# Kernel optimization log

Hardware: AMD Instinct MI355X
Metric: run time of the kernel (lower is better)

## Reference

```python
import jax, jax.numpy as jnp
import numpy as np

V, E, H = 50000, 300, 512
L, N, K = 6, 8192, 4


def setup_inputs() -> dict:
    key = jax.random.key(0)
    ks = jax.random.split(key, 12)
    vocab_ix = jax.random.randint(ks[0], (L, N), 0, V)
    child_idx = jax.random.randint(ks[1], (L, N, K), 0, N)
    token_mask = jnp.ones((L, N), dtype=jnp.float32)
    child_mask = (jax.random.uniform(ks[2], (L, N, K)) < 0.75).astype(jnp.float32)
    s = 0.02
    embed = jax.random.normal(ks[3], (V, E), dtype=jnp.float32)
    W_iou = jax.random.normal(ks[4], (E, 3 * H), dtype=jnp.float32) * s
    U_iou = jax.random.normal(ks[5], (H, 3 * H), dtype=jnp.float32) * s
    b_iou = jnp.zeros((3 * H,), dtype=jnp.float32)
    W_f = jax.random.normal(ks[6], (E, H), dtype=jnp.float32) * s
    U_f = jax.random.normal(ks[7], (H, H), dtype=jnp.float32) * s
    b_f = jnp.zeros((H,), dtype=jnp.float32)
    return {"vocab_ix": vocab_ix, "child_idx": child_idx, "token_mask": token_mask,
            "child_mask": child_mask, "embed": embed, "W_iou": W_iou, "U_iou": U_iou,
            "b_iou": b_iou, "W_f": W_f, "U_f": U_f, "b_f": b_f}


def _tree_lstm(vocab_ix, child_idx, token_mask, child_mask,
               embed, W_iou, U_iou, b_iou, W_f, U_f, b_f):
    # bottom-up over levels; level L-1 = leaves (no children -> zero prev states)
    h = jnp.zeros((N, H), dtype=embed.dtype)
    c = jnp.zeros((N, H), dtype=embed.dtype)
    for l in reversed(range(L)):
        # word2vec: embedding lookup; zero vector for non-token nodes
        x = embed[vocab_ix[l]] * token_mask[l][:, None]            # [N, E]
        xWf = x @ W_f                                              # [N, H]
        if l == L - 1:
            h_tilde = jnp.zeros((N, H), dtype=x.dtype)
            fc = jnp.zeros((N, H), dtype=x.dtype)
        else:
            m = child_mask[l][:, :, None]                          # [N, K, 1]
            h_ch = h[child_idx[l]] * m                             # [N, K, H]
            c_ch = c[child_idx[l]] * m                             # [N, K, H]
            h_tilde = h_ch.sum(axis=1)                             # child-sum
            # per-child forget gates (padded slots: c_ch is 0 -> no contribution)
            f = jax.nn.sigmoid(xWf[:, None, :] + jnp.einsum('nkh,hj->nkj', h_ch, U_f) + b_f)
            fc = (f * c_ch).sum(axis=1)
        iou = x @ W_iou + h_tilde @ U_iou + b_iou                  # [N, 3H]
        i, o, u = jnp.split(iou, 3, axis=-1)
        c = jax.nn.sigmoid(i) * jnp.tanh(u) + fc
        h = jax.nn.sigmoid(o) * jnp.tanh(c)
    return h  # outputs[0][1]: hidden states of root level


def reference(vocab_ix, child_idx, token_mask, child_mask,
              embed, W_iou, U_iou, b_iou, W_f, U_f, b_f):
    return _tree_lstm(vocab_ix, child_idx, token_mask, child_mask,
                      embed, W_iou, U_iou, b_iou, W_f, U_f, b_f)
```

## Files before the change

kernel.cpp:

```cpp
#include <hip/hip_runtime.h>
#include <cmath>

#define VSZ  50000
#define EDIM 300
#define EPAD 320
#define HDIM 512
#define LVLS 6
#define NN   8192
#define KCH  4

#define BM 128
#define BN 128
#define BK 32

typedef __attribute__((ext_vector_type(8))) short bf16x8;
typedef __attribute__((ext_vector_type(8))) unsigned short us8;
typedef __attribute__((ext_vector_type(4))) float f32x4;

__device__ __forceinline__ float sigf(float x) { return 1.0f / (1.0f + expf(-x)); }

__device__ __forceinline__ unsigned short f2bf(float f) {
    unsigned u = __float_as_uint(f);
    u += 0x7FFF + ((u >> 16) & 1);
    return (unsigned short)(u >> 16);
}
__device__ __forceinline__ float bf2f(unsigned short h) {
    return __uint_as_float(((unsigned)h) << 16);
}

__device__ __forceinline__ unsigned cvt_pk_bf16(float lo, float hi) {
    unsigned r;
    asm("v_cvt_pk_bf16_f32 %0, %1, %2" : "=v"(r) : "v"(lo), "v"(hi));
    return r;
}

__global__ __launch_bounds__(256) void gconv_k(
    const float* __restrict__ embed, const int* __restrict__ vix,
    const float* __restrict__ tmask, unsigned short* __restrict__ out)
{
    int t  = blockIdx.x * 256 + threadIdx.x;
    int r  = t / (EPAD / 8);
    int j8 = (t - r * (EPAD / 8)) * 8;
    float m = tmask[r];
    int   v = vix[r];
    const float* src = embed + (size_t)v * EDIM + j8;
    us8 o;
    if (j8 + 8 <= EDIM) {
        float4 a = *(const float4*)(src);
        float4 b = *(const float4*)(src + 4);
        const float xs[8] = {a.x, a.y, a.z, a.w, b.x, b.y, b.z, b.w};
#pragma unroll
        for (int j = 0; j < 8; ++j) o[j] = f2bf(xs[j] * m);
    } else {
#pragma unroll
        for (int j = 0; j < 8; ++j) {
            float x = (j8 + j < EDIM) ? src[j] * m : 0.0f;
            o[j] = f2bf(x);
        }
    }
    *(us8*)(out + (size_t)r * EPAD + j8) = o;
}

__global__ __launch_bounds__(256) void wconv_k(
    const float* __restrict__ in, unsigned short* __restrict__ out,
    int Kreal, int Ksp, int Nd)
{
    int t = blockIdx.x * 256 + threadIdx.x;
    int k = t % Ksp;
    int n = t / Ksp;
    out[t] = (k < Kreal) ? f2bf(in[(size_t)k * Nd + n]) : (unsigned short)0;
}

#define GLL(src, dst)                                                        \
    __builtin_amdgcn_global_load_lds(                                        \
        (const __attribute__((address_space(1))) unsigned int*)(src), (dst), 16, 0, 0)

template <int EPI, int NCHUNK>
__global__ __launch_bounds__(256) void mgemm_k(
    const unsigned short* __restrict__ Ab,
    const unsigned short* __restrict__ Bt,
    const float* __restrict__ b_iou, const float* __restrict__ b_f,
    unsigned short* __restrict__ C, int ldc, int Ks)
{
    __shared__ __align__(16) unsigned short smem[4 * BM * BK];
    unsigned short* As0 = smem;
    unsigned short* Bs0 = smem + BM * BK;
    unsigned short* As1 = smem + 2 * BM * BK;
    unsigned short* Bs1 = smem + 3 * BM * BK;

    const int tid  = threadIdx.x;
    const int wave = tid >> 6;
    const int lane = tid & 63;
    const int quad = lane >> 4;
    const int mcol = lane & 15;
    const int wm   = (wave >> 1) * 64;
    const int wn   = (wave & 1) * 64;
    const int band = wave >> 1;

    const int GX   = gridDim.x;
    const int P    = blockIdx.x + GX * blockIdx.y;
    const int g    = P & 7;
    const int s    = P >> 3;
    const int mper = gridDim.y >> 3;
    const int sdiv = s / GX;
    const int my_mt = g * mper + sdiv;
    const int my_ng = s - sdiv * GX;
    const int tile_m = my_mt * BM;

    const int r0  = tid >> 2;
    const int kg0 = (tid & 3) ^ ((r0 >> 1) & 3);
    const int cc1 = tid + 256;
    const int r1  = cc1 >> 2;
    const int kg1 = (cc1 & 3) ^ ((r1 >> 1) & 3);

    const unsigned short* asrc0 = Ab + (size_t)(tile_m + r0) * Ks + kg0 * 8;
    const unsigned short* asrc1 = Ab + (size_t)(tile_m + r1) * Ks + kg1 * 8;

    typedef __attribute__((address_space(3))) unsigned int lds_u32;
    lds_u32* dA0_0 = (lds_u32*)(As0 + wave * 512);
    lds_u32* dA1_0 = (lds_u32*)(As0 + 2048 + wave * 512);
    lds_u32* dB0_0 = (lds_u32*)(Bs0 + wave * 512);
    lds_u32* dB1_0 = (lds_u32*)(Bs0 + 2048 + wave * 512);
    lds_u32* dA0_1 = (lds_u32*)(As1 + wave * 512);
    lds_u32* dA1_1 = (lds_u32*)(As1 + 2048 + wave * 512);
    lds_u32* dB0_1 = (lds_u32*)(Bs1 + wave * 512);
    lds_u32* dB1_1 = (lds_u32*)(Bs1 + 2048 + wave * 512);

    float* eb = reinterpret_cast<float*>(smem);
    const int erl = tid >> 3;
    const int ecg = tid & 7;

#define STAGE0(kk) { GLL(asrc0 + (kk), dA0_0); GLL(asrc1 + (kk), dA1_0);    \
                     GLL(bsrc0 + (kk), dB0_0); GLL(bsrc1 + (kk), dB1_0); }
#define STAGE1(kk) { GLL(asrc0 + (kk), dA0_1); GLL(asrc1 + (kk), dA1_1);    \
                     GLL(bsrc0 + (kk), dB0_1); GLL(bsrc1 + (kk), dB1_1); }
#define WAITV4  asm volatile("s_waitcnt vmcnt(4)" ::: "memory")
#define WAITV0  asm volatile("s_waitcnt vmcnt(0)" ::: "memory")
#define BAR     __builtin_amdgcn_s_barrier()

#define COMPUTE(AS, BS)                                                     \
    {                                                                       \
        bf16x8 afr[4], bfr[4];                                              \
        _Pragma("unroll")                                                   \
        for (int mt = 0; mt < 4; ++mt) {                                    \
            int rw = wm + mt * 16 + mcol;                                   \
            int p  = rw * 4 + (quad ^ ((rw >> 1) & 3));                     \
            afr[mt] = *(const bf16x8*)((AS) + p * 8);                       \
        }                                                                   \
        _Pragma("unroll")                                                   \
        for (int nt = 0; nt < 4; ++nt) {                                    \
            int rw = wn + nt * 16 + mcol;                                   \
            int p  = rw * 4 + (quad ^ ((rw >> 1) & 3));                     \
            bfr[nt] = *(const bf16x8*)((BS) + p * 8);                       \
        }                                                                   \
        _Pragma("unroll")                                                   \
        for (int mt = 0; mt < 4; ++mt)                                      \
            _Pragma("unroll")                                               \
            for (int nt = 0; nt < 4; ++nt)                                  \
                acc[mt][nt] = __builtin_amdgcn_mfma_f32_16x16x32_bf16(      \
                    afr[mt], bfr[nt], acc[mt][nt], 0, 0, 0);                \
    }

    for (int nc = 0; nc < NCHUNK; ++nc) {
        const int tile_n = (my_ng * NCHUNK + nc) * BN;
        const unsigned short* bsrc0 = Bt + (size_t)(tile_n + r0) * Ks + kg0 * 8;
        const unsigned short* bsrc1 = Bt + (size_t)(tile_n + r1) * Ks + kg1 * 8;

        f32x4 acc[4][4] = {};
        const int nsteps = Ks / BK;

        STAGE0(0);

        for (int st = 0; st < nsteps; st += 2) {
            if (st + 1 < nsteps) { STAGE1((st + 1) * BK); WAITV4; }
            else                 { WAITV0; }
            BAR;
            COMPUTE(As0, Bs0);
            BAR;
            if (st + 2 < nsteps) { STAGE0((st + 2) * BK); WAITV4; }
            else                 { WAITV0; }
            BAR;
            COMPUTE(As1, Bs1);
            BAR;
        }

#pragma unroll
        for (int mt = 0; mt < 4; ++mt) {
            const int rbase = band * 16 + quad * 4;
#pragma unroll
            for (int nt = 0; nt < 4; ++nt) {
                const int cb = wn + nt * 16 + mcol;
                const int gq = cb >> 2;
                const int cl = cb & 3;
#pragma unroll
                for (int rr = 0; rr < 4; ++rr) {
                    const int r = rbase + rr;
                    eb[r * 128 + ((gq ^ (r & 7)) << 2) + cl] = acc[mt][nt][rr];
                }
            }
            __syncthreads();

            const int grow = tile_m + (erl >> 4) * 64 + mt * 16 + (erl & 15);
            const int gcol = tile_n + ecg * 16;
            float v[16];
#pragma unroll
            for (int sxt = 0; sxt < 4; ++sxt) {
                const int pg = (ecg * 4 + sxt) ^ (erl & 7);
                f32x4 q = *(const f32x4*)&eb[erl * 128 + pg * 4];
                v[sxt * 4 + 0] = q[0]; v[sxt * 4 + 1] = q[1];
                v[sxt * 4 + 2] = q[2]; v[sxt * 4 + 3] = q[3];
            }
            if (EPI == 1) {
                const float* bp = (gcol < 3 * HDIM) ? (b_iou + gcol)
                                                    : (b_f + gcol - 3 * HDIM);
                float4 b0 = *(const float4*)(bp);
                float4 b1 = *(const float4*)(bp + 4);
                float4 b2 = *(const float4*)(bp + 8);
                float4 b3 = *(const float4*)(bp + 12);
                const float bb[16] = {b0.x, b0.y, b0.z, b0.w, b1.x, b1.y, b1.z, b1.w,
                                      b2.x, b2.y, b2.z, b2.w, b3.x, b3.y, b3.z, b3.w};
#pragma unroll
                for (int j = 0; j < 16; ++j) v[j] += bb[j];
            }
            unsigned pw[8];
#pragma unroll
            for (int j = 0; j < 8; ++j) pw[j] = cvt_pk_bf16(v[2 * j], v[2 * j + 1]);
            unsigned short* cp = C + (size_t)grow * ldc + gcol;
            *(uint4*)(cp)     = make_uint4(pw[0], pw[1], pw[2], pw[3]);
            *(uint4*)(cp + 8) = make_uint4(pw[4], pw[5], pw[6], pw[7]);
            __syncthreads();
        }
    }
#undef STAGE0
#undef STAGE1
#undef WAITV4
#undef WAITV0
#undef BAR
#undef COMPUTE
}

template <bool LAST>
__global__ __launch_bounds__(256) void gatefc_k(
    const unsigned short* __restrict__ iouxW, const unsigned short* __restrict__ Z,
    const int* __restrict__ cidx, const float* __restrict__ cmask,
    const float* __restrict__ c_prev,
    float* __restrict__ c_new, unsigned short* __restrict__ hb_new,
    float* __restrict__ h_out)
{
    int t  = blockIdx.x * 256 + threadIdx.x;
    int n  = t >> 6;
    int j8 = (t & 63) << 3;
    const unsigned short* xr = iouxW + (size_t)n * 4 * HDIM + j8;
    us8 xi = *(const us8*)xr;
    us8 xo = *(const us8*)(xr + HDIM);
    us8 xu = *(const us8*)(xr + 2 * HDIM);
    us8 xf = *(const us8*)(xr + 3 * HDIM);
    float ia[8], oa[8], ua[8], xw[8], fc[8];
#pragma unroll
    for (int j = 0; j < 8; ++j) {
        ia[j] = bf2f(xi[j]); oa[j] = bf2f(xo[j]);
        ua[j] = bf2f(xu[j]); xw[j] = bf2f(xf[j]);
        fc[j] = 0.0f;
    }
    int4   ci = *(const int4*)&cidx[n * KCH];
    float4 cm = *(const float4*)&cmask[n * KCH];
    const int   cia[4] = {ci.x, ci.y, ci.z, ci.w};
    const float cma[4] = {cm.x, cm.y, cm.z, cm.w};
#pragma unroll
    for (int k = 0; k < KCH; ++k) {
        const float m = cma[k];
        const unsigned short* zr = Z + (size_t)cia[k] * 4 * HDIM + j8;
        us8 zi = *(const us8*)zr;
        us8 zo = *(const us8*)(zr + HDIM);
        us8 zu = *(const us8*)(zr + 2 * HDIM);
        us8 zf = *(const us8*)(zr + 3 * HDIM);
        const float* cpr = c_prev + (size_t)cia[k] * HDIM + j8;
        float4 ca = *(const float4*)cpr;
        float4 cb = *(const float4*)(cpr + 4);
        const float cp[8] = {ca.x, ca.y, ca.z, ca.w, cb.x, cb.y, cb.z, cb.w};
#pragma unroll
        for (int j = 0; j < 8; ++j) {
            ia[j] += m * bf2f(zi[j]);
            oa[j] += m * bf2f(zo[j]);
            ua[j] += m * bf2f(zu[j]);
            fc[j] += sigf(xw[j] + m * bf2f(zf[j])) * m * cp[j];
        }
    }
    float cv[8], hv[8];
#pragma unroll
    for (int j = 0; j < 8; ++j) {
        cv[j] = sigf(ia[j]) * tanhf(ua[j]) + fc[j];
        hv[j] = sigf(oa[j]) * tanhf(cv[j]);
    }
    if (LAST) {
        float4 h0 = make_float4(hv[0], hv[1], hv[2], hv[3]);
        float4 h1 = make_float4(hv[4], hv[5], hv[6], hv[7]);
        *(float4*)(h_out + (size_t)n * HDIM + j8)     = h0;
        *(float4*)(h_out + (size_t)n * HDIM + j8 + 4) = h1;
    } else {
        float4 c0v = make_float4(cv[0], cv[1], cv[2], cv[3]);
        float4 c1v = make_float4(cv[4], cv[5], cv[6], cv[7]);
        *(float4*)(c_new + (size_t)n * HDIM + j8)     = c0v;
        *(float4*)(c_new + (size_t)n * HDIM + j8 + 4) = c1v;
        us8 hb;
#pragma unroll
        for (int j = 0; j < 8; ++j) hb[j] = f2bf(hv[j]);
        *(us8*)(hb_new + (size_t)n * HDIM + j8) = hb;
    }
}

__global__ __launch_bounds__(256) void gateleaf_k(
    const unsigned short* __restrict__ iouxW,
    float* __restrict__ c_new, unsigned short* __restrict__ hb_new)
{
    int t  = blockIdx.x * 256 + threadIdx.x;
    int n  = t >> 6;
    int j8 = (t & 63) << 3;
    const unsigned short* xr = iouxW + (size_t)n * 4 * HDIM + j8;
    us8 xi = *(const us8*)xr;
    us8 xo = *(const us8*)(xr + HDIM);
    us8 xu = *(const us8*)(xr + 2 * HDIM);
    float cv[8], hv[8];
#pragma unroll
    for (int j = 0; j < 8; ++j) {
        cv[j] = sigf(bf2f(xi[j])) * tanhf(bf2f(xu[j]));
        hv[j] = sigf(bf2f(xo[j])) * tanhf(cv[j]);
    }
    float4 c0v = make_float4(cv[0], cv[1], cv[2], cv[3]);
    float4 c1v = make_float4(cv[4], cv[5], cv[6], cv[7]);
    *(float4*)(c_new + (size_t)n * HDIM + j8)     = c0v;
    *(float4*)(c_new + (size_t)n * HDIM + j8 + 4) = c1v;
    us8 hb;
#pragma unroll
    for (int j = 0; j < 8; ++j) hb[j] = f2bf(hv[j]);
    *(us8*)(hb_new + (size_t)n * HDIM + j8) = hb;
}

extern "C" void kernel_launch(void* const* d_in, const int* in_sizes, int n_in,
                              void* d_out, int out_size, void* d_ws, size_t ws_size,
                              hipStream_t stream)
{
    const int*   vocab_ix   = (const int*)d_in[0];
    const int*   child_idx  = (const int*)d_in[1];
    const float* token_mask = (const float*)d_in[2];
    const float* child_mask = (const float*)d_in[3];
    const float* embed      = (const float*)d_in[4];
    const float* W_iou      = (const float*)d_in[5];
    const float* U_iou      = (const float*)d_in[6];
    const float* b_iou      = (const float*)d_in[7];
    const float* W_f        = (const float*)d_in[8];
    const float* U_f        = (const float*)d_in[9];
    const float* b_f        = (const float*)d_in[10];
    float* out = (float*)d_out;

    float* ws = (float*)d_ws;
    float* c0 = ws;
    float* c1 = c0 + (size_t)NN * HDIM;
    unsigned short* usb   = (unsigned short*)(c1 + (size_t)NN * HDIM);
    unsigned short* hb0   = usb;
    unsigned short* hb1   = hb0 + (size_t)NN * HDIM;
    unsigned short* iouxW = hb1 + (size_t)NN * HDIM;
    unsigned short* Z     = iouxW + (size_t)3 * NN * 4 * HDIM;
    unsigned short* AbatA = Z + (size_t)NN * 4 * HDIM;
    unsigned short* AbatB = AbatA + (size_t)3 * NN * EPAD;
    unsigned short* WtALL = AbatB + (size_t)3 * NN * EPAD;
    unsigned short* UtALL = WtALL + (size_t)4 * HDIM * EPAD;

    dim3 blk(256);

    const int grows = 3 * NN * (EPAD / 8) / 256;
    gconv_k<<<dim3(grows), blk, 0, stream>>>(embed, vocab_ix + (size_t)3 * NN,
                                             token_mask + (size_t)3 * NN, AbatA);
    gconv_k<<<dim3(grows), blk, 0, stream>>>(embed, vocab_ix, token_mask, AbatB);
    wconv_k<<<dim3(3 * HDIM * EPAD / 256), blk, 0, stream>>>(W_iou, WtALL, EDIM, EPAD, 3 * HDIM);
    wconv_k<<<dim3(HDIM * EPAD / 256),     blk, 0, stream>>>(W_f, WtALL + (size_t)3 * HDIM * EPAD, EDIM, EPAD, HDIM);
    wconv_k<<<dim3(3 * HDIM * HDIM / 256), blk, 0, stream>>>(U_iou, UtALL, HDIM, HDIM, 3 * HDIM);
    wconv_k<<<dim3(HDIM * HDIM / 256),     blk, 0, stream>>>(U_f, UtALL + (size_t)3 * HDIM * HDIM, HDIM, HDIM, HDIM);

    unsigned short* bbuf[2] = { hb0, hb1 };
    float*          cbuf[2] = { c0,  c1  };

    const int ew_blocks = NN * HDIM / 8 / 256;

    mgemm_k<1, 2><<<dim3(8, 3 * NN / BM), blk, 0, stream>>>(
        AbatA, WtALL, b_iou, b_f, iouxW, 4 * HDIM, EPAD);

    for (int l = LVLS - 1; l >= 0; --l) {
        const int p = (LVLS - 1 - l);
        unsigned short* hb_new  = bbuf[p & 1];
        float*          c_new   = cbuf[p & 1];
        unsigned short* hb_prev = bbuf[(p & 1) ^ 1];
        float*          c_prev  = cbuf[(p & 1) ^ 1];
        const int*   cix = child_idx  + (size_t)l * NN * KCH;
        const float* cm  = child_mask + (size_t)l * NN * KCH;
        const unsigned short* ix_l =
            iouxW + (size_t)((l >= 3) ? (l - 3) : l) * NN * 4 * HDIM;

        if (l == LVLS - 1) {
            gateleaf_k<<<dim3(ew_blocks), blk, 0, stream>>>(ix_l, c_new, hb_new);
        } else {
            mgemm_k<0, 2><<<dim3(8, NN / BM), blk, 0, stream>>>(
                hb_prev, UtALL, nullptr, nullptr, Z, 4 * HDIM, HDIM);

            if (l == 0) {
                gatefc_k<true><<<dim3(ew_blocks), blk, 0, stream>>>(
                    ix_l, Z, cix, cm, c_prev, nullptr, nullptr, out);
            } else {
                gatefc_k<false><<<dim3(ew_blocks), blk, 0, stream>>>(
                    ix_l, Z, cix, cm, c_prev, c_new, hb_new, nullptr);
            }
        }

        if (l == 3) {
            mgemm_k<1, 2><<<dim3(8, 3 * NN / BM), blk, 0, stream>>>(
                AbatB, WtALL, b_iou, b_f, iouxW, 4 * HDIM, EPAD);
        }
    }
}
```

Baseline: 603.2 us.

## Switch GEMM main loop to triple-buffered LDS with one barrier per step

Replaces the double-buffered A/B shared-memory staging with a three-slot rotating ring. The load for step st+2 is issued before computing step st. Each K-step now needs only one barrier instead of two, and loads get more lead time to hide global-memory latency. LDS use per block rises from 32KB to 48KB, which may lower occupancy. The rotating buffer offsets are runtime values, which may add address arithmetic.

```diff
diff --git a/kernel.cpp b/kernel.cpp
--- a/kernel.cpp
+++ b/kernel.cpp
@@ -82,11 +82,7 @@
     const float* __restrict__ b_iou, const float* __restrict__ b_f,
     unsigned short* __restrict__ C, int ldc, int Ks)
 {
-    __shared__ __align__(16) unsigned short smem[4 * BM * BK];
-    unsigned short* As0 = smem;
-    unsigned short* Bs0 = smem + BM * BK;
-    unsigned short* As1 = smem + 2 * BM * BK;
-    unsigned short* Bs1 = smem + 3 * BM * BK;
+    __shared__ __align__(16) unsigned short smem[6 * BM * BK];
 
     const int tid  = threadIdx.x;
     const int wave = tid >> 6;
@@ -117,41 +113,38 @@
     const unsigned short* asrc1 = Ab + (size_t)(tile_m + r1) * Ks + kg1 * 8;
 
     typedef __attribute__((address_space(3))) unsigned int lds_u32;
-    lds_u32* dA0_0 = (lds_u32*)(As0 + wave * 512);
-    lds_u32* dA1_0 = (lds_u32*)(As0 + 2048 + wave * 512);
-    lds_u32* dB0_0 = (lds_u32*)(Bs0 + wave * 512);
-    lds_u32* dB1_0 = (lds_u32*)(Bs0 + 2048 + wave * 512);
-    lds_u32* dA0_1 = (lds_u32*)(As1 + wave * 512);
-    lds_u32* dA1_1 = (lds_u32*)(As1 + 2048 + wave * 512);
-    lds_u32* dB0_1 = (lds_u32*)(Bs1 + wave * 512);
-    lds_u32* dB1_1 = (lds_u32*)(Bs1 + 2048 + wave * 512);
 
     float* eb = reinterpret_cast<float*>(smem);
     const int erl = tid >> 3;
     const int ecg = tid & 7;
 
-#define STAGE0(kk) { GLL(asrc0 + (kk), dA0_0); GLL(asrc1 + (kk), dA1_0);    \
-                     GLL(bsrc0 + (kk), dB0_0); GLL(bsrc1 + (kk), dB1_0); }
-#define STAGE1(kk) { GLL(asrc0 + (kk), dA0_1); GLL(asrc1 + (kk), dA1_1);    \
-                     GLL(bsrc0 + (kk), dB0_1); GLL(bsrc1 + (kk), dB1_1); }
+#define STAGE3(kk, bo)                                                       \
+    {                                                                        \
+        GLL(asrc0 + (kk), (lds_u32*)(smem + (bo) + wave * 512));             \
+        GLL(asrc1 + (kk), (lds_u32*)(smem + (bo) + 2048 + wave * 512));      \
+        GLL(bsrc0 + (kk), (lds_u32*)(smem + (bo) + 4096 + wave * 512));      \
+        GLL(bsrc1 + (kk), (lds_u32*)(smem + (bo) + 6144 + wave * 512));      \
+    }
 #define WAITV4  asm volatile("s_waitcnt vmcnt(4)" ::: "memory")
 #define WAITV0  asm volatile("s_waitcnt vmcnt(0)" ::: "memory")
 #define BAR     __builtin_amdgcn_s_barrier()
 
-#define COMPUTE(AS, BS)                                                     \
+#define COMPUTE(bo)                                                         \
     {                                                                       \
+        const unsigned short* AS = smem + (bo);                             \
+        const unsigned short* BS = smem + (bo) + 4096;                      \
         bf16x8 afr[4], bfr[4];                                              \
         _Pragma("unroll")                                                   \
         for (int mt = 0; mt < 4; ++mt) {                                    \
             int rw = wm + mt * 16 + mcol;                                   \
             int p  = rw * 4 + (quad ^ ((rw >> 1) & 3));                     \
-            afr[mt] = *(const bf16x8*)((AS) + p * 8);                       \
+            afr[mt] = *(const bf16x8*)(AS + p * 8);                         \
         }                                                                   \
         _Pragma("unroll")                                                   \
         for (int nt = 0; nt < 4; ++nt) {                                    \
             int rw = wn + nt * 16 + mcol;                                   \
             int p  = rw * 4 + (quad ^ ((rw >> 1) & 3));                     \
-            bfr[nt] = *(const bf16x8*)((BS) + p * 8);                       \
+            bfr[nt] = *(const bf16x8*)(BS + p * 8);                         \
         }                                                                   \
         _Pragma("unroll")                                                   \
         for (int mt = 0; mt < 4; ++mt)                                      \
@@ -169,19 +162,20 @@
         f32x4 acc[4][4] = {};
         const int nsteps = Ks / BK;
 
-        STAGE0(0);
-
-        for (int st = 0; st < nsteps; st += 2) {
-            if (st + 1 < nsteps) { STAGE1((st + 1) * BK); WAITV4; }
-            else                 { WAITV0; }
+        int bo0 = 0, bo1 = 8192, bo2 = 16384;
+
+        STAGE3(0, bo0);
+        STAGE3(BK, bo1);
+        WAITV4;
+        BAR;
+
+        for (int st = 0; st < nsteps; ++st) {
+            const bool pf = (st + 2 < nsteps);
+            if (pf) STAGE3((st + 2) * BK, bo2);
+            COMPUTE(bo0);
+            if (pf) { WAITV4; } else { WAITV0; }
             BAR;
-            COMPUTE(As0, Bs0);
-            BAR;
-            if (st + 2 < nsteps) { STAGE0((st + 2) * BK); WAITV4; }
-            else                 { WAITV0; }
-            BAR;
-            COMPUTE(As1, Bs1);
-            BAR;
+            int t0 = bo0; bo0 = bo1; bo1 = bo2; bo2 = t0;
         }
 
 #pragma unroll
@@ -231,8 +225,7 @@
             __syncthreads();
         }
     }
-#undef STAGE0
-#undef STAGE1
+#undef STAGE3
 #undef WAITV4
 #undef WAITV0
 #undef BAR
```

After: 598.5 us. No clear change (-0.8%).
